# Performance work log

Hardware: AMD Instinct MI355X
Metric: run time of the kernel (lower is better)

## Reference

```python
import jax, jax.numpy as jnp
import numpy as np

RADIUS = 0.1          # acceptance_radius
CONF = 0.2            # confidence_threshold
MIN_LOCAL = 3         # min_local_correspondences
MIN_GLOBAL = 256      # min_global_correspondences
STEPS = 5             # num_refinement_steps
EPS = 1e-5
NTH = 8               # candidate thresholds CONF - 0.05*k (replaces data-dependent while loop)


def weighted_procrustes(src, tgt, w):
    """Weighted Kabsch. src/tgt: (..., N, 3), w: (..., N). Returns R (...,3,3), t (...,3)."""
    w = w / (jnp.sum(w, axis=-1, keepdims=True) + EPS)
    src_c = jnp.einsum('...n,...nc->...c', w, src)
    tgt_c = jnp.einsum('...n,...nc->...c', w, tgt)
    s0 = src - src_c[..., None, :]
    t0 = tgt - tgt_c[..., None, :]
    H = jnp.einsum('...nc,...n,...nd->...cd', s0, w, t0)  # (...,3,3)
    U, S, Vt = jnp.linalg.svd(H)
    V = jnp.swapaxes(Vt, -1, -2)
    det = jnp.linalg.det(jnp.matmul(V, jnp.swapaxes(U, -1, -2)))
    d = jnp.stack([jnp.ones_like(det), jnp.ones_like(det), det], axis=-1)
    R = jnp.einsum('...ik,...k,...jk->...ij', V, d, U)
    t = tgt_c - jnp.einsum('...ij,...j->...i', R, src_c)
    return R, t


def setup_inputs() -> dict:
    key = jax.random.key(0)
    k0, k1, k2 = jax.random.split(key, 3)
    B, K = 128, 64
    src = jax.random.normal(k0, (B, K, 3), dtype=jnp.float32)
    tgt = jax.random.normal(k1, (B, K, 3), dtype=jnp.float32)
    score_mat = jax.random.normal(k2, (B, K, K), dtype=jnp.float32) * 2.0 - 4.0
    src_masks = jnp.ones((B, K), dtype=bool)
    tgt_masks = jnp.ones((B, K), dtype=bool)
    return {
        'src_knn_points': src,
        'tgt_knn_points': tgt,
        'src_knn_masks': src_masks,
        'tgt_knn_masks': tgt_masks,
        'score_mat': score_mat,
    }


def reference(src_knn_points, tgt_knn_points, src_knn_masks, tgt_knn_masks, score_mat):
    B, K, _ = score_mat.shape
    score = jax.nn.sigmoid(score_mat)
    mask = src_knn_masks[:, :, None] & tgt_knn_masks[:, None, :]  # (B,K,K)

    # --- threshold search (dense replacement for the while loop) ---
    mg = jnp.minimum(min(3 * K, MIN_GLOBAL), jnp.sum(mask))
    th = CONF - 0.05 * jnp.arange(NTH, dtype=score.dtype)
    cnts = jnp.sum((score[None] > th[:, None, None, None]) & mask[None], axis=(1, 2, 3))
    thr = th[jnp.argmax(cnts >= mg)]  # first threshold with enough correspondences

    corr = (score > thr) & mask          # dense corr_mat (B,K,K)
    score = score * corr.astype(score.dtype)

    # --- dense (masked) correspondence batching: all (i,j) pairs per patch ---
    srcP = jnp.broadcast_to(src_knn_points[:, :, None, :], (B, K, K, 3)).reshape(B, K * K, 3)
    tgtP = jnp.broadcast_to(tgt_knn_points[:, None, :, :], (B, K, K, 3)).reshape(B, K * K, 3)
    w = score.reshape(B, K * K)

    # per-patch hypothesis transforms (zero-weight pairs are ignored by Procrustes)
    Rb, tb = weighted_procrustes(srcP, tgtP, w)  # (B,3,3), (B,3)
    counts_b = jnp.sum(corr, axis=(1, 2))
    valid = counts_b >= MIN_LOCAL

    # --- hypothesis verification: inlier counts over all global correspondences ---
    aligned = jnp.einsum('bxy,piy->bpix', Rb, src_knn_points) + tb[:, None, None, :]  # (B,B,K,3)
    cross = jnp.einsum('bpix,pjx->bpij', aligned, tgt_knn_points)                     # (B,B,K,K)
    res2 = (jnp.sum(aligned ** 2, -1)[..., None]
            + jnp.sum(tgt_knn_points ** 2, -1)[None, :, None, :]
            - 2.0 * cross)
    inlier = (res2 < RADIUS ** 2) & corr[None]                                        # (B,B,K,K)
    cnt_T = jnp.where(valid, jnp.sum(inlier, axis=(1, 2, 3)), -1)
    best = jnp.argmax(cnt_T)

    cur = score * inlier[best].astype(score.dtype)

    # --- global refinement ---
    src_all = srcP.reshape(-1, 3)
    tgt_all = tgtP.reshape(-1, 3)
    score_all = score.reshape(-1)
    R, t = weighted_procrustes(src_all, tgt_all, cur.reshape(-1))
    for _ in range(STEPS - 1):
        res = jnp.linalg.norm(tgt_all - (src_all @ R.T + t), axis=-1)
        cur_all = score_all * (res < RADIUS).astype(score.dtype)
        R, t = weighted_procrustes(src_all, tgt_all, cur_all)

    estimated_transform = jnp.eye(4, dtype=score.dtype).at[:3, :3].set(R).at[:3, 3].set(t)
    return estimated_transform, score  # score = dense-masked correspondence scores (B,K,K)
```

## Files before the change

### kernel.cpp

```cpp
#include <hip/hip_runtime.h>
#include <math.h>

#define BB   128
#define KK   64
#define K2   (KK*KK)
#define NTH  8
#define MG   192
#define MIN_LOCAL 3
#define RADIUS2 0.01f
#define RADIUSF 0.1f
#define NW   8

static constexpr size_t OFF_CNT8S = 0;
static constexpr size_t OFF_MA    = 0;
static constexpr size_t OFF_CNTU  = 8192;
static constexpr size_t OFF_MB    = 8192;
static constexpr size_t OFF_VALID = 40960;
static constexpr size_t OFF_RB    = 41472;
static constexpr size_t OFF_CB    = 47616;

__device__ inline void eigvec3(const double A[3][3], double lambda, double v[3]) {
    double r0x = A[0][0] - lambda, r0y = A[0][1], r0z = A[0][2];
    double r1x = A[0][1], r1y = A[1][1] - lambda, r1z = A[1][2];
    double r2x = A[0][2], r2y = A[1][2], r2z = A[2][2] - lambda;
    double c0x = r0y * r1z - r0z * r1y, c0y = r0z * r1x - r0x * r1z, c0z = r0x * r1y - r0y * r1x;
    double c1x = r0y * r2z - r0z * r2y, c1y = r0z * r2x - r0x * r2z, c1z = r0x * r2y - r0y * r2x;
    double c2x = r1y * r2z - r1z * r2y, c2y = r1z * r2x - r1x * r2z, c2z = r1x * r2y - r1y * r2x;
    double n0 = c0x * c0x + c0y * c0y + c0z * c0z;
    double n1 = c1x * c1x + c1y * c1y + c1z * c1z;
    double n2 = c2x * c2x + c2y * c2y + c2z * c2z;
    double bx = c0x, by = c0y, bz = c0z, nb = n0;
    if (n1 > nb) { bx = c1x; by = c1y; bz = c1z; nb = n1; }
    if (n2 > nb) { bx = c2x; by = c2y; bz = c2z; nb = n2; }
    if (nb < 1e-280) { v[0] = 1.0; v[1] = 0.0; v[2] = 0.0; return; }
    double s = 1.0 / sqrt(nb);
    v[0] = bx * s; v[1] = by * s; v[2] = bz * s;
}

__device__ inline void eig3(const double A[3][3], double V[3][3], double lam[3]) {
    double q = (A[0][0] + A[1][1] + A[2][2]) / 3.0;
    double a00 = A[0][0] - q, a11 = A[1][1] - q, a22 = A[2][2] - q;
    double p1 = A[0][1] * A[0][1] + A[0][2] * A[0][2] + A[1][2] * A[1][2];
    double p2 = a00 * a00 + a11 * a11 + a22 * a22 + 2.0 * p1;
    if (p2 < 1e-280) {
        lam[0] = q; lam[1] = q; lam[2] = q;
        for (int i = 0; i < 3; i++)
            for (int j = 0; j < 3; j++) V[i][j] = (i == j) ? 1.0 : 0.0;
        return;
    }
    double p = sqrt(p2 / 6.0);
    double ip = 1.0 / p;
    double b00 = a00 * ip, b11 = a11 * ip, b22 = a22 * ip;
    double b01 = A[0][1] * ip, b02 = A[0][2] * ip, b12 = A[1][2] * ip;
    double detB = b00 * (b11 * b22 - b12 * b12)
                - b01 * (b01 * b22 - b12 * b02)
                + b02 * (b01 * b12 - b11 * b02);
    double r = 0.5 * detB;
    r = fmin(1.0, fmax(-1.0, r));
    double phi = acos(r) / 3.0;
    double l0 = q + 2.0 * p * cos(phi);
    double l2 = q + 2.0 * p * cos(phi + 2.0943951023931953);
    double l1 = 3.0 * q - l0 - l2;
    lam[0] = l0; lam[1] = l1; lam[2] = l2;

    double v0[3], v2[3];
    eigvec3(A, l0, v0);
    eigvec3(A, l2, v2);
    double d = v0[0] * v2[0] + v0[1] * v2[1] + v0[2] * v2[2];
    v2[0] -= d * v0[0]; v2[1] -= d * v0[1]; v2[2] -= d * v0[2];
    double n = v2[0] * v2[0] + v2[1] * v2[1] + v2[2] * v2[2];
    if (n < 1e-280) {
        int k = (fabs(v0[0]) <= fabs(v0[1]) && fabs(v0[0]) <= fabs(v0[2])) ? 0
              : ((fabs(v0[1]) <= fabs(v0[2])) ? 1 : 2);
        double ax[3] = {0.0, 0.0, 0.0}; ax[k] = 1.0;
        double dd = v0[k];
        v2[0] = ax[0] - dd * v0[0]; v2[1] = ax[1] - dd * v0[1]; v2[2] = ax[2] - dd * v0[2];
        n = v2[0] * v2[0] + v2[1] * v2[1] + v2[2] * v2[2];
    }
    double s2 = 1.0 / sqrt(n);
    v2[0] *= s2; v2[1] *= s2; v2[2] *= s2;
    double v1[3] = { v2[1] * v0[2] - v2[2] * v0[1],
                     v2[2] * v0[0] - v2[0] * v0[2],
                     v2[0] * v0[1] - v2[1] * v0[0] };
    for (int i = 0; i < 3; i++) { V[i][0] = v0[i]; V[i][1] = v1[i]; V[i][2] = v2[i]; }
}

__device__ inline void kabsch_from_moments(const double* m, double R[3][3], double t[3]) {
    double W = m[0];
    double denom = W + 1e-5;
    double s = W / denom;
    double sc[3], tc[3];
    for (int c = 0; c < 3; c++) { sc[c] = m[1 + c] / denom; tc[c] = m[4 + c] / denom; }
    double H[3][3];
    for (int c = 0; c < 3; c++)
        for (int d = 0; d < 3; d++)
            H[c][d] = m[7 + c * 3 + d] / denom - (2.0 - s) * sc[c] * tc[d];
    double B3[3][3];
    for (int i = 0; i < 3; i++)
        for (int j = 0; j < 3; j++) {
            double v = 0.0;
            for (int k = 0; k < 3; k++) v += H[k][i] * H[k][j];
            B3[i][j] = v;
        }
    double V[3][3], lam[3];
    eig3(B3, V, lam);
    double inv[3];
    for (int k = 0; k < 3; k++) {
        double sg = sqrt(fmax(lam[k], 0.0));
        inv[k] = (sg > 1e-150) ? 1.0 / sg : 0.0;
    }
    double detH = H[0][0] * (H[1][1] * H[2][2] - H[1][2] * H[2][1])
                - H[0][1] * (H[1][0] * H[2][2] - H[1][2] * H[2][0])
                + H[0][2] * (H[1][0] * H[2][1] - H[1][1] * H[2][0]);
    if (detH < 0.0) inv[2] = -inv[2];
    double T2[3][3];
    for (int i = 0; i < 3; i++)
        for (int j = 0; j < 3; j++) {
            double v = 0.0;
            for (int k = 0; k < 3; k++) v += V[i][k] * inv[k] * V[j][k];
            T2[i][j] = v;
        }
    for (int i = 0; i < 3; i++)
        for (int j = 0; j < 3; j++) {
            double v = 0.0;
            for (int k = 0; k < 3; k++) v += T2[i][k] * H[j][k];
            R[i][j] = v;
        }
    for (int i = 0; i < 3; i++) {
        double v = tc[i];
        for (int j = 0; j < 3; j++) v -= R[i][j] * sc[j];
        t[i] = v;
    }
}

__global__ __launch_bounds__(512) void k_counts(
    const float* __restrict__ sm, int* __restrict__ cnt8s)
{
    const int t = threadIdx.x, lane = t & 63, wave = t >> 6;
    const int b = blockIdx.x;
    __shared__ int sC8[NTH];
    float xv[8];
    #pragma unroll
    for (int u = 0; u < 8; u++)
        xv[u] = sm[b * K2 + (u * NW + wave) * KK + lane];
    if (t < NTH) sC8[t] = 0;
    __syncthreads();
    int ck[NTH];
    #pragma unroll
    for (int k = 0; k < NTH; k++) ck[k] = 0;
    for (int u = 0; u < 8; u++) {
        float s = 1.0f / (1.0f + expf(-xv[u]));
        #pragma unroll
        for (int k = 0; k < NTH; k++) {
            unsigned long long bal = __ballot(s > (0.2f - 0.05f * (float)k));
            ck[k] += (int)__popcll(bal);
        }
    }
    if (lane == 0) {
        #pragma unroll
        for (int k = 0; k < NTH; k++) atomicAdd(&sC8[k], ck[k]);
    }
    __syncthreads();
    if (t < NTH) cnt8s[b * NTH + t] = sC8[t];
}

__global__ __launch_bounds__(512) void k_local(
    const float* __restrict__ src, const float* __restrict__ tgt,
    const float* __restrict__ sm, const int* __restrict__ cnt8s,
    float* __restrict__ score, unsigned long long* __restrict__ corrb,
    float* __restrict__ Rb, int* __restrict__ validA)
{
    const int t = threadIdx.x, lane = t & 63, wave = t >> 6;
    const int b = blockIdx.x;
    __shared__ float sS[192];
    __shared__ float sT[256];
    __shared__ float sRed[NW * 16];
    __shared__ int sRedi[NW];
    __shared__ float sThr;

    float xv[8];
    #pragma unroll
    for (int u = 0; u < 8; u++)
        xv[u] = sm[b * K2 + (u * NW + wave) * KK + lane];
    if (t < 192) sS[t] = src[b * 192 + t];
    if (t < 64) {
        float x = tgt[b * 192 + t * 3], y = tgt[b * 192 + t * 3 + 1], z = tgt[b * 192 + t * 3 + 2];
        sT[t * 4] = x; sT[t * 4 + 1] = y; sT[t * 4 + 2] = z; sT[t * 4 + 3] = x * x + y * y + z * z;
    }
    if (wave == 0) {
        int a[NTH];
        #pragma unroll
        for (int k = 0; k < NTH; k++)
            a[k] = cnt8s[lane * NTH + k] + cnt8s[(lane + 64) * NTH + k];
        #pragma unroll
        for (int off = 32; off; off >>= 1)
            #pragma unroll
            for (int k = 0; k < NTH; k++) a[k] += __shfl_down(a[k], off);
        if (lane == 0) {
            int kk2 = 0; bool found = false;
            #pragma unroll
            for (int k = 0; k < NTH; k++)
                if (!found && a[k] >= MG) { kk2 = k; found = true; }
            sThr = 0.2f - 0.05f * (float)kk2;
        }
    }
    __syncthreads();

    float thr = sThr;
    float tx0 = sT[lane * 4], ty0 = sT[lane * 4 + 1], tz0 = sT[lane * 4 + 2];
    float acc[16];
    #pragma unroll
    for (int k = 0; k < 16; k++) acc[k] = 0.0f;
    int cnt = 0;
    for (int u = 0; u < 8; u++) {
        int i = u * NW + wave;
        float s = 1.0f / (1.0f + expf(-xv[u]));
        bool c = (s > thr);
        float w = c ? s : 0.0f;
        score[b * K2 + i * KK + lane] = w;
        unsigned long long bal = __ballot(c);
        if (lane == 0) corrb[b * KK + i] = bal;
        cnt += c ? 1 : 0;
        float sx = sS[i * 3], sy = sS[i * 3 + 1], sz = sS[i * 3 + 2];
        acc[0]  += w;
        acc[1]  += w * sx; acc[2]  += w * sy; acc[3]  += w * sz;
        acc[4]  += w * tx0; acc[5]  += w * ty0; acc[6]  += w * tz0;
        acc[7]  += w * sx * tx0; acc[8]  += w * sx * ty0; acc[9]  += w * sx * tz0;
        acc[10] += w * sy * tx0; acc[11] += w * sy * ty0; acc[12] += w * sy * tz0;
        acc[13] += w * sz * tx0; acc[14] += w * sz * ty0; acc[15] += w * sz * tz0;
    }
    #pragma unroll
    for (int off = 32; off; off >>= 1) {
        #pragma unroll
        for (int k = 0; k < 16; k++) acc[k] += __shfl_down(acc[k], off);
        cnt += __shfl_down(cnt, off);
    }
    if (lane == 0) {
        for (int k = 0; k < 16; k++) sRed[wave * 16 + k] = acc[k];
        sRedi[wave] = cnt;
    }
    __syncthreads();
    if (t == 0) {
        double m[16];
        for (int k = 0; k < 16; k++) {
            float v = 0.0f;
            for (int wv = 0; wv < NW; wv++) v += sRed[wv * 16 + k];
            m[k] = (double)v;
        }
        double R[3][3], tv[3];
        kabsch_from_moments(m, R, tv);
        for (int i = 0; i < 3; i++)
            for (int j = 0; j < 3; j++) Rb[b * 12 + i * 3 + j] = (float)R[i][j];
        for (int i = 0; i < 3; i++) Rb[b * 12 + 9 + i] = (float)tv[i];
        int ctot = 0;
        for (int wv = 0; wv < NW; wv++) ctot += sRedi[wv];
        validA[b] = (ctot >= MIN_LOCAL) ? 1 : 0;
    }
}

__global__ __launch_bounds__(512) void k_verify(
    const float* __restrict__ src, const float* __restrict__ tgt,
    const unsigned long long* __restrict__ corrb, const float* __restrict__ Rb,
    unsigned int* __restrict__ cntU)
{
    const int t = threadIdx.x, lane = t & 63, wave = t >> 6;
    const int unit = blockIdx.x;
    const int p = unit >> 2, b0 = (unit & 3) * 32;
    __shared__ float sT[256];
    __shared__ float sRT[384];
    __shared__ int sCnt[32];

    if (t < 64) {
        float x = tgt[p * 192 + t * 3], y = tgt[p * 192 + t * 3 + 1], z = tgt[p * 192 + t * 3 + 2];
        sT[t * 4] = x; sT[t * 4 + 1] = y; sT[t * 4 + 2] = z; sT[t * 4 + 3] = x * x + y * y + z * z;
    }
    if (t < 384) sRT[t] = Rb[b0 * 12 + t];
    float sx = src[p * 192 + lane * 3];
    float sy = src[p * 192 + lane * 3 + 1];
    float sz = src[p * 192 + lane * 3 + 2];
    unsigned long long mask = corrb[p * KK + lane];
    __syncthreads();

    float ax[4], ay[4], az[4], sa[4];
    #pragma unroll
    for (int k = 0; k < 4; k++) {
        const float* RT = &sRT[(wave * 4 + k) * 12];
        ax[k] = RT[0] * sx + RT[1] * sy + RT[2] * sz + RT[9];
        ay[k] = RT[3] * sx + RT[4] * sy + RT[5] * sz + RT[10];
        az[k] = RT[6] * sx + RT[7] * sy + RT[8] * sz + RT[11];
        sa[k] = ax[k] * ax[k] + ay[k] * ay[k] + az[k] * az[k];
    }
    int c[4] = {0, 0, 0, 0};
    const float4* sT4 = (const float4*)sT;
    unsigned long long s = mask;
    while (s) {
        int j = (int)__builtin_ctzll(s);
        s &= s - 1ULL;
        float4 tv = sT4[j];
        #pragma unroll
        for (int k = 0; k < 4; k++) {
            float d2 = (sa[k] + tv.w) - 2.0f * (ax[k] * tv.x + ay[k] * tv.y + az[k] * tv.z);
            c[k] += (d2 < RADIUS2) ? 1 : 0;
        }
    }
    #pragma unroll
    for (int off = 32; off; off >>= 1)
        #pragma unroll
        for (int k = 0; k < 4; k++) c[k] += __shfl_down(c[k], off);
    if (lane == 0) {
        #pragma unroll
        for (int k = 0; k < 4; k++) sCnt[wave * 4 + k] = c[k];
    }
    __syncthreads();
    if (t < 16) {
        unsigned int pk = ((unsigned int)sCnt[2 * t] & 0xFFFFu)
                        | ((unsigned int)sCnt[2 * t + 1] << 16);
        cntU[unit * 16 + t] = pk;
    }
}

__device__ inline void refine_moments(
    const float* sS, const float* sT, const float* sRTf, float* sAl,
    const float* wv8, int t, int lane, int wave, bool it0,
    float* sRed)
{
    if (t < 64) {
        float x = sS[t * 3], y = sS[t * 3 + 1], z = sS[t * 3 + 2];
        float ax = sRTf[0] * x + sRTf[1] * y + sRTf[2] * z + sRTf[9];
        float ay = sRTf[3] * x + sRTf[4] * y + sRTf[5] * z + sRTf[10];
        float az = sRTf[6] * x + sRTf[7] * y + sRTf[8] * z + sRTf[11];
        sAl[t * 4] = ax; sAl[t * 4 + 1] = ay; sAl[t * 4 + 2] = az;
        sAl[t * 4 + 3] = ax * ax + ay * ay + az * az;
    }
    __syncthreads();
    float tx = sT[lane * 4], ty = sT[lane * 4 + 1], tz = sT[lane * 4 + 2], st2 = sT[lane * 4 + 3];
    float acc[16];
    #pragma unroll
    for (int k = 0; k < 16; k++) acc[k] = 0.0f;
    for (int u = 0; u < 8; u++) {
        int i = u * NW + wave;
        float sx = sS[i * 3], sy = sS[i * 3 + 1], sz = sS[i * 3 + 2];
        float ax = sAl[i * 4], ay = sAl[i * 4 + 1], az = sAl[i * 4 + 2], sa = sAl[i * 4 + 3];
        bool pred;
        if (it0) {
            float d2 = (sa + st2) - 2.0f * (ax * tx + ay * ty + az * tz);
            pred = (d2 < RADIUS2);
        } else {
            float dx = tx - ax, dy = ty - ay, dz = tz - az;
            pred = (sqrtf(dx * dx + dy * dy + dz * dz) < RADIUSF);
        }
        float w = wv8[u];
        float wf = pred ? w : 0.0f;
        acc[0]  += wf;
        acc[1]  += wf * sx; acc[2]  += wf * sy; acc[3]  += wf * sz;
        acc[4]  += wf * tx; acc[5]  += wf * ty; acc[6]  += wf * tz;
        acc[7]  += wf * sx * tx; acc[8]  += wf * sx * ty; acc[9]  += wf * sx * tz;
        acc[10] += wf * sy * tx; acc[11] += wf * sy * ty; acc[12] += wf * sy * tz;
        acc[13] += wf * sz * tx; acc[14] += wf * sz * ty; acc[15] += wf * sz * tz;
    }
    #pragma unroll
    for (int off = 32; off; off >>= 1)
        #pragma unroll
        for (int k = 0; k < 16; k++) acc[k] += __shfl_down(acc[k], off);
    if (lane == 0)
        for (int k = 0; k < 16; k++) sRed[wave * 16 + k] = acc[k];
}

__global__ __launch_bounds__(512) void k_sel_it0(
    const float* __restrict__ src, const float* __restrict__ tgt,
    const unsigned int* __restrict__ cntU, const int* __restrict__ validA,
    const float* __restrict__ Rb, const float* __restrict__ score,
    float* __restrict__ mout)
{
    const int t = threadIdx.x, lane = t & 63, wave = t >> 6;
    const int b = blockIdx.x;
    __shared__ float sS[192];
    __shared__ float sT[256];
    __shared__ float sAl[256];
    __shared__ float sRed[NW * 16];
    __shared__ int sCT[BB], sVv[BB];
    __shared__ int sCTp[512];
    __shared__ float sRTf[12];
    __shared__ int sBest;

    float wv8[8];
    #pragma unroll
    for (int u = 0; u < 8; u++)
        wv8[u] = score[b * K2 + (u * NW + wave) * KK + lane];
    if (t < 192) sS[t] = src[b * 192 + t];
    if (t < 64) {
        float x = tgt[b * 192 + t * 3], y = tgt[b * 192 + t * 3 + 1], z = tgt[b * 192 + t * 3 + 2];
        sT[t * 4] = x; sT[t * 4 + 1] = y; sT[t * 4 + 2] = z; sT[t * 4 + 3] = x * x + y * y + z * z;
    }
    {
        int q = t >> 7, h = t & 127;
        int g = h >> 5, w = (h & 31) >> 1, sh = (h & 1) * 16;
        int ssum = 0;
        for (int p = q * 32; p < q * 32 + 32; p++) {
            unsigned int wv = cntU[(p * 4 + g) * 16 + w];
            ssum += (int)((wv >> sh) & 0xFFFFu);
        }
        sCTp[t] = ssum;
    }
    __syncthreads();
    if (t < BB) {
        sCT[t] = sCTp[t] + sCTp[t + 128] + sCTp[t + 256] + sCTp[t + 384];
        sVv[t] = validA[t];
    }
    __syncthreads();
    if (t == 0) {
        int best = 0, bc = -2;
        for (int bb = 0; bb < BB; bb++) {
            int c = sVv[bb] ? sCT[bb] : -1;
            if (c > bc) { bc = c; best = bb; }
        }
        sBest = best;
    }
    __syncthreads();
    if (t < 12) sRTf[t] = Rb[sBest * 12 + t];
    __syncthreads();

    refine_moments(sS, sT, sRTf, sAl, wv8, t, lane, wave, true, sRed);
    __syncthreads();
    if (t < 16) {
        float v = 0.0f;
        for (int wv = 0; wv < NW; wv++) v += sRed[wv * 16 + t];
        mout[b * 16 + t] = v;
    }
}

__global__ __launch_bounds__(512) void k_refine(
    const float* __restrict__ src, const float* __restrict__ tgt,
    const float* __restrict__ score, const float* __restrict__ min_,
    float* __restrict__ mout)
{
    const int t = threadIdx.x, lane = t & 63, wave = t >> 6;
    const int b = blockIdx.x;
    __shared__ float sS[192];
    __shared__ float sT[256];
    __shared__ float sAl[256];
    __shared__ float sRed[NW * 16];
    __shared__ double sRTd[12];
    __shared__ float sRTf[12];

    float wv8[8];
    #pragma unroll
    for (int u = 0; u < 8; u++)
        wv8[u] = score[b * K2 + (u * NW + wave) * KK + lane];
    if (t < 192) sS[t] = src[b * 192 + t];
    if (t < 64) {
        float x = tgt[b * 192 + t * 3], y = tgt[b * 192 + t * 3 + 1], z = tgt[b * 192 + t * 3 + 2];
        sT[t * 4] = x; sT[t * 4 + 1] = y; sT[t * 4 + 2] = z; sT[t * 4 + 3] = x * x + y * y + z * z;
    }
    if (wave == 0) {
        double a[16];
        #pragma unroll
        for (int k = 0; k < 16; k++)
            a[k] = (double)min_[lane * 16 + k] + (double)min_[(lane + 64) * 16 + k];
        #pragma unroll
        for (int off = 32; off; off >>= 1)
            #pragma unroll
            for (int k = 0; k < 16; k++) a[k] += __shfl_down(a[k], off);
        if (lane == 0) {
            double R[3][3], tv[3];
            kabsch_from_moments(a, R, tv);
            for (int i = 0; i < 3; i++)
                for (int j = 0; j < 3; j++) sRTd[i * 3 + j] = R[i][j];
            for (int i = 0; i < 3; i++) sRTd[9 + i] = tv[i];
        }
    }
    __syncthreads();
    if (t < 12) sRTf[t] = (float)sRTd[t];
    __syncthreads();

    refine_moments(sS, sT, sRTf, sAl, wv8, t, lane, wave, false, sRed);
    __syncthreads();
    if (t < 16) {
        float v = 0.0f;
        for (int wv = 0; wv < NW; wv++) v += sRed[wv * 16 + t];
        mout[b * 16 + t] = v;
    }
}

__global__ __launch_bounds__(64) void k_final(
    const float* __restrict__ min_, float* __restrict__ out)
{
    const int lane = threadIdx.x;
    double a[16];
    #pragma unroll
    for (int k = 0; k < 16; k++)
        a[k] = (double)min_[lane * 16 + k] + (double)min_[(lane + 64) * 16 + k];
    #pragma unroll
    for (int off = 32; off; off >>= 1)
        #pragma unroll
        for (int k = 0; k < 16; k++) a[k] += __shfl_down(a[k], off);
    if (lane == 0) {
        double R[3][3], tv[3];
        kabsch_from_moments(a, R, tv);
        for (int i = 0; i < 3; i++) {
            for (int j = 0; j < 3; j++) out[i * 4 + j] = (float)R[i][j];
            out[i * 4 + 3] = (float)tv[i];
        }
        out[12] = 0.0f; out[13] = 0.0f; out[14] = 0.0f; out[15] = 1.0f;
    }
}

extern "C" void kernel_launch(void* const* d_in, const int* in_sizes, int n_in,
                              void* d_out, int out_size, void* d_ws, size_t ws_size,
                              hipStream_t stream) {
    const float* src = (const float*)d_in[0];
    const float* tgt = (const float*)d_in[1];
    const float* sm  = (const float*)d_in[4];
    float* out = (float*)d_out;
    char* ws = (char*)d_ws;

    int* cnt8s   = (int*)(ws + OFF_CNT8S);
    unsigned int* cntU = (unsigned int*)(ws + OFF_CNTU);
    float* mA    = (float*)(ws + OFF_MA);
    float* mB    = (float*)(ws + OFF_MB);
    int* validA  = (int*)(ws + OFF_VALID);
    float* Rb    = (float*)(ws + OFF_RB);
    unsigned long long* corrb = (unsigned long long*)(ws + OFF_CB);
    float* score = out + 16;

    k_counts <<<BB, 512, 0, stream>>>(sm, cnt8s);
    k_local  <<<BB, 512, 0, stream>>>(src, tgt, sm, cnt8s, score, corrb, Rb, validA);
    k_verify <<<512, 512, 0, stream>>>(src, tgt, corrb, Rb, cntU);
    k_sel_it0<<<BB, 512, 0, stream>>>(src, tgt, cntU, validA, Rb, score, mA);
    k_refine <<<BB, 512, 0, stream>>>(src, tgt, score, mA, mB);
    k_refine <<<BB, 512, 0, stream>>>(src, tgt, score, mB, mA);
    k_refine <<<BB, 512, 0, stream>>>(src, tgt, score, mA, mB);
    k_refine <<<BB, 512, 0, stream>>>(src, tgt, score, mB, mA);
    k_final  <<<1, 64, 0, stream>>>(mA, out);
}
```

Before: 145.0 us.

## Fuse refinement iterations into one persistent kernel with grid-wide spin barriers

Replaces the selection kernel, the four refine launches and the final reduction with a single 8-block persistent kernel. Each block handles 16 batches and publishes per-iteration moment sums through atomics and tags. All blocks spin-wait on those tags, then recompute Kabsch redundantly. This removes about six kernel launches and their gaps, at the cost of using only 8 CUs for the refinement work. It also relies on all 8 blocks being co-resident and on a timeout-guarded spin barrier.

New measurement: 364.4 us. 2.51x slower.

```diff
diff --git a/kernel.cpp b/kernel.cpp
--- a/kernel.cpp
+++ b/kernel.cpp
@@ -10,14 +10,16 @@
 #define RADIUS2 0.01f
 #define RADIUSF 0.1f
 #define NW   8
+#define NRB  8
+#define AGT  __HIP_MEMORY_SCOPE_AGENT
 
 static constexpr size_t OFF_CNT8S = 0;
-static constexpr size_t OFF_MA    = 0;
-static constexpr size_t OFF_CNTU  = 8192;
-static constexpr size_t OFF_MB    = 8192;
-static constexpr size_t OFF_VALID = 40960;
-static constexpr size_t OFF_RB    = 41472;
-static constexpr size_t OFF_CB    = 47616;
+static constexpr size_t OFF_CNTU  = 4096;
+static constexpr size_t OFF_VALID = 36864;
+static constexpr size_t OFF_RB    = 37376;
+static constexpr size_t OFF_CB    = 43520;
+static constexpr size_t OFF_TAGR  = 109056;
+static constexpr size_t OFF_MSD   = 109120;
 
 __device__ inline void eigvec3(const double A[3][3], double lambda, double v[3]) {
     double r0x = A[0][0] - lambda, r0y = A[0][1], r0z = A[0][2];
@@ -131,6 +133,23 @@
         for (int j = 0; j < 3; j++) v -= R[i][j] * sc[j];
         t[i] = v;
     }
+}
+
+__device__ inline void wait8(const int* tagR, int lane, int val) {
+    int spins = 0;
+    unsigned long long t0 = 0;
+    for (;;) {
+        bool ok = (lane >= NRB) ||
+                  (__hip_atomic_load(&tagR[lane], __ATOMIC_RELAXED, AGT) >= val);
+        if (__ballot(ok) == ~0ULL) break;
+        if (spins > 16) __builtin_amdgcn_s_sleep(1);
+        if ((++spins & 63) == 0) {
+            unsigned long long now = __builtin_amdgcn_s_memrealtime();
+            if (t0 == 0) t0 = now;
+            else if (__ballot(now - t0 > 10000000ULL) != 0ULL) break;
+        }
+    }
+    __atomic_signal_fence(__ATOMIC_SEQ_CST);
 }
 
 __global__ __launch_bounds__(512) void k_counts(
@@ -261,7 +280,7 @@
 __global__ __launch_bounds__(512) void k_verify(
     const float* __restrict__ src, const float* __restrict__ tgt,
     const unsigned long long* __restrict__ corrb, const float* __restrict__ Rb,
-    unsigned int* __restrict__ cntU)
+    unsigned int* __restrict__ cntU, int* __restrict__ tagR)
 {
     const int t = threadIdx.x, lane = t & 63, wave = t >> 6;
     const int unit = blockIdx.x;
@@ -270,6 +289,7 @@
     __shared__ float sRT[384];
     __shared__ int sCnt[32];
 
+    if (unit == 0 && t < 16) tagR[t] = 0;
     if (t < 64) {
         float x = tgt[p * 192 + t * 3], y = tgt[p * 192 + t * 3 + 1], z = tgt[p * 192 + t * 3 + 2];
         sT[t * 4] = x; sT[t * 4 + 1] = y; sT[t * 4 + 2] = z; sT[t * 4 + 3] = x * x + y * y + z * z;
@@ -319,79 +339,37 @@
     }
 }
 
-__device__ inline void refine_moments(
-    const float* sS, const float* sT, const float* sRTf, float* sAl,
-    const float* wv8, int t, int lane, int wave, bool it0,
-    float* sRed)
-{
-    if (t < 64) {
-        float x = sS[t * 3], y = sS[t * 3 + 1], z = sS[t * 3 + 2];
-        float ax = sRTf[0] * x + sRTf[1] * y + sRTf[2] * z + sRTf[9];
-        float ay = sRTf[3] * x + sRTf[4] * y + sRTf[5] * z + sRTf[10];
-        float az = sRTf[6] * x + sRTf[7] * y + sRTf[8] * z + sRTf[11];
-        sAl[t * 4] = ax; sAl[t * 4 + 1] = ay; sAl[t * 4 + 2] = az;
-        sAl[t * 4 + 3] = ax * ax + ay * ay + az * az;
-    }
-    __syncthreads();
-    float tx = sT[lane * 4], ty = sT[lane * 4 + 1], tz = sT[lane * 4 + 2], st2 = sT[lane * 4 + 3];
-    float acc[16];
-    #pragma unroll
-    for (int k = 0; k < 16; k++) acc[k] = 0.0f;
-    for (int u = 0; u < 8; u++) {
-        int i = u * NW + wave;
-        float sx = sS[i * 3], sy = sS[i * 3 + 1], sz = sS[i * 3 + 2];
-        float ax = sAl[i * 4], ay = sAl[i * 4 + 1], az = sAl[i * 4 + 2], sa = sAl[i * 4 + 3];
-        bool pred;
-        if (it0) {
-            float d2 = (sa + st2) - 2.0f * (ax * tx + ay * ty + az * tz);
-            pred = (d2 < RADIUS2);
-        } else {
-            float dx = tx - ax, dy = ty - ay, dz = tz - az;
-            pred = (sqrtf(dx * dx + dy * dy + dz * dz) < RADIUSF);
-        }
-        float w = wv8[u];
-        float wf = pred ? w : 0.0f;
-        acc[0]  += wf;
-        acc[1]  += wf * sx; acc[2]  += wf * sy; acc[3]  += wf * sz;
-        acc[4]  += wf * tx; acc[5]  += wf * ty; acc[6]  += wf * tz;
-        acc[7]  += wf * sx * tx; acc[8]  += wf * sx * ty; acc[9]  += wf * sx * tz;
-        acc[10] += wf * sy * tx; acc[11] += wf * sy * ty; acc[12] += wf * sy * tz;
-        acc[13] += wf * sz * tx; acc[14] += wf * sz * ty; acc[15] += wf * sz * tz;
-    }
-    #pragma unroll
-    for (int off = 32; off; off >>= 1)
-        #pragma unroll
-        for (int k = 0; k < 16; k++) acc[k] += __shfl_down(acc[k], off);
-    if (lane == 0)
-        for (int k = 0; k < 16; k++) sRed[wave * 16 + k] = acc[k];
-}
-
-__global__ __launch_bounds__(512) void k_sel_it0(
+__global__ __launch_bounds__(512) void k_refineall(
     const float* __restrict__ src, const float* __restrict__ tgt,
-    const unsigned int* __restrict__ cntU, const int* __restrict__ validA,
-    const float* __restrict__ Rb, const float* __restrict__ score,
-    float* __restrict__ mout)
+    const float* __restrict__ score, const unsigned int* __restrict__ cntU,
+    const int* __restrict__ validA, const float* __restrict__ Rb,
+    int* __restrict__ tagR, double* __restrict__ msd, float* __restrict__ out)
 {
     const int t = threadIdx.x, lane = t & 63, wave = t >> 6;
-    const int b = blockIdx.x;
-    __shared__ float sS[192];
-    __shared__ float sT[256];
-    __shared__ float sAl[256];
-    __shared__ float sRed[NW * 16];
+    const int blk = blockIdx.x;
+
+    __shared__ float sSp[16 * 192];
+    __shared__ float sTp[16 * 256];
+    __shared__ float sAl[16 * 256];
+    __shared__ float sRedAll[16 * 8 * 16];
+    __shared__ float sPm[16 * 16];
+    __shared__ double sMdL[16];
     __shared__ int sCT[BB], sVv[BB];
     __shared__ int sCTp[512];
+    __shared__ double sRTd[12];
     __shared__ float sRTf[12];
     __shared__ int sBest;
 
-    float wv8[8];
-    #pragma unroll
-    for (int u = 0; u < 8; u++)
-        wv8[u] = score[b * K2 + (u * NW + wave) * KK + lane];
-    if (t < 192) sS[t] = src[b * 192 + t];
-    if (t < 64) {
-        float x = tgt[b * 192 + t * 3], y = tgt[b * 192 + t * 3 + 1], z = tgt[b * 192 + t * 3 + 2];
-        sT[t * 4] = x; sT[t * 4 + 1] = y; sT[t * 4 + 2] = z; sT[t * 4 + 3] = x * x + y * y + z * z;
-    }
+    for (int idx = t; idx < 16 * 192; idx += 512)
+        sSp[idx] = src[blk * 16 * 192 + idx];
+    for (int idx = t; idx < 1024; idx += 512) {
+        int p = idx >> 6, i = idx & 63;
+        const float* tp = tgt + (blk * 16 + p) * 192 + i * 3;
+        float x = tp[0], y = tp[1], z = tp[2];
+        sTp[idx * 4] = x; sTp[idx * 4 + 1] = y; sTp[idx * 4 + 2] = z;
+        sTp[idx * 4 + 3] = x * x + y * y + z * z;
+    }
+
     {
         int q = t >> 7, h = t & 127;
         int g = h >> 5, w = (h & 31) >> 1, sh = (h & 1) * 16;
@@ -420,88 +398,119 @@
     if (t < 12) sRTf[t] = Rb[sBest * 12 + t];
     __syncthreads();
 
-    refine_moments(sS, sT, sRTf, sAl, wv8, t, lane, wave, true, sRed);
-    __syncthreads();
-    if (t < 16) {
-        float v = 0.0f;
-        for (int wv = 0; wv < NW; wv++) v += sRed[wv * 16 + t];
-        mout[b * 16 + t] = v;
-    }
-}
-
-__global__ __launch_bounds__(512) void k_refine(
-    const float* __restrict__ src, const float* __restrict__ tgt,
-    const float* __restrict__ score, const float* __restrict__ min_,
-    float* __restrict__ mout)
-{
-    const int t = threadIdx.x, lane = t & 63, wave = t >> 6;
-    const int b = blockIdx.x;
-    __shared__ float sS[192];
-    __shared__ float sT[256];
-    __shared__ float sAl[256];
-    __shared__ float sRed[NW * 16];
-    __shared__ double sRTd[12];
-    __shared__ float sRTf[12];
-
-    float wv8[8];
-    #pragma unroll
-    for (int u = 0; u < 8; u++)
-        wv8[u] = score[b * K2 + (u * NW + wave) * KK + lane];
-    if (t < 192) sS[t] = src[b * 192 + t];
-    if (t < 64) {
-        float x = tgt[b * 192 + t * 3], y = tgt[b * 192 + t * 3 + 1], z = tgt[b * 192 + t * 3 + 2];
-        sT[t * 4] = x; sT[t * 4 + 1] = y; sT[t * 4 + 2] = z; sT[t * 4 + 3] = x * x + y * y + z * z;
-    }
-    if (wave == 0) {
-        double a[16];
-        #pragma unroll
-        for (int k = 0; k < 16; k++)
-            a[k] = (double)min_[lane * 16 + k] + (double)min_[(lane + 64) * 16 + k];
-        #pragma unroll
-        for (int off = 32; off; off >>= 1)
+    for (int it = 0; it < 5; it++) {
+        for (int idx = t; idx < 1024; idx += 512) {
+            int p = idx >> 6, i = idx & 63;
+            float x = sSp[p * 192 + i * 3], y = sSp[p * 192 + i * 3 + 1], z = sSp[p * 192 + i * 3 + 2];
+            float ax = sRTf[0] * x + sRTf[1] * y + sRTf[2] * z + sRTf[9];
+            float ay = sRTf[3] * x + sRTf[4] * y + sRTf[5] * z + sRTf[10];
+            float az = sRTf[6] * x + sRTf[7] * y + sRTf[8] * z + sRTf[11];
+            sAl[idx * 4] = ax; sAl[idx * 4 + 1] = ay; sAl[idx * 4 + 2] = az;
+            sAl[idx * 4 + 3] = ax * ax + ay * ay + az * az;
+        }
+        __syncthreads();
+        for (int p = 0; p < 16; p++) {
+            float tx = sTp[(p * 64 + lane) * 4],     ty = sTp[(p * 64 + lane) * 4 + 1];
+            float tz = sTp[(p * 64 + lane) * 4 + 2], st2 = sTp[(p * 64 + lane) * 4 + 3];
+            const float* scp = score + (blk * 16 + p) * K2;
+            float acc[16];
             #pragma unroll
-            for (int k = 0; k < 16; k++) a[k] += __shfl_down(a[k], off);
-        if (lane == 0) {
-            double R[3][3], tv[3];
-            kabsch_from_moments(a, R, tv);
-            for (int i = 0; i < 3; i++)
-                for (int j = 0; j < 3; j++) sRTd[i * 3 + j] = R[i][j];
-            for (int i = 0; i < 3; i++) sRTd[9 + i] = tv[i];
-        }
-    }
-    __syncthreads();
-    if (t < 12) sRTf[t] = (float)sRTd[t];
-    __syncthreads();
-
-    refine_moments(sS, sT, sRTf, sAl, wv8, t, lane, wave, false, sRed);
-    __syncthreads();
-    if (t < 16) {
-        float v = 0.0f;
-        for (int wv = 0; wv < NW; wv++) v += sRed[wv * 16 + t];
-        mout[b * 16 + t] = v;
-    }
-}
-
-__global__ __launch_bounds__(64) void k_final(
-    const float* __restrict__ min_, float* __restrict__ out)
-{
-    const int lane = threadIdx.x;
-    double a[16];
-    #pragma unroll
-    for (int k = 0; k < 16; k++)
-        a[k] = (double)min_[lane * 16 + k] + (double)min_[(lane + 64) * 16 + k];
-    #pragma unroll
-    for (int off = 32; off; off >>= 1)
-        #pragma unroll
-        for (int k = 0; k < 16; k++) a[k] += __shfl_down(a[k], off);
-    if (lane == 0) {
-        double R[3][3], tv[3];
-        kabsch_from_moments(a, R, tv);
-        for (int i = 0; i < 3; i++) {
-            for (int j = 0; j < 3; j++) out[i * 4 + j] = (float)R[i][j];
-            out[i * 4 + 3] = (float)tv[i];
-        }
-        out[12] = 0.0f; out[13] = 0.0f; out[14] = 0.0f; out[15] = 1.0f;
+            for (int k = 0; k < 16; k++) acc[k] = 0.0f;
+            for (int u = 0; u < 8; u++) {
+                int i = u * NW + wave;
+                float w = scp[i * KK + lane];
+                float sx = sSp[p * 192 + i * 3], sy = sSp[p * 192 + i * 3 + 1], sz = sSp[p * 192 + i * 3 + 2];
+                int ai = (p * 64 + i) * 4;
+                float ax = sAl[ai], ay = sAl[ai + 1], az = sAl[ai + 2], sa = sAl[ai + 3];
+                bool pred;
+                if (it == 0) {
+                    float d2 = (sa + st2) - 2.0f * (ax * tx + ay * ty + az * tz);
+                    pred = (d2 < RADIUS2);
+                } else {
+                    float dx = tx - ax, dy = ty - ay, dz = tz - az;
+                    pred = (sqrtf(dx * dx + dy * dy + dz * dz) < RADIUSF);
+                }
+                float wf = pred ? w : 0.0f;
+                acc[0]  += wf;
+                acc[1]  += wf * sx; acc[2]  += wf * sy; acc[3]  += wf * sz;
+                acc[4]  += wf * tx; acc[5]  += wf * ty; acc[6]  += wf * tz;
+                acc[7]  += wf * sx * tx; acc[8]  += wf * sx * ty; acc[9]  += wf * sx * tz;
+                acc[10] += wf * sy * tx; acc[11] += wf * sy * ty; acc[12] += wf * sy * tz;
+                acc[13] += wf * sz * tx; acc[14] += wf * sz * ty; acc[15] += wf * sz * tz;
+            }
+            #pragma unroll
+            for (int off = 32; off; off >>= 1)
+                #pragma unroll
+                for (int k = 0; k < 16; k++) acc[k] += __shfl_down(acc[k], off);
+            if (lane == 0)
+                for (int k = 0; k < 16; k++) sRedAll[(p * 8 + wave) * 16 + k] = acc[k];
+        }
+        __syncthreads();
+        if (t < 256) {
+            int p = t >> 4, k = t & 15;
+            float v = 0.0f;
+            for (int wv = 0; wv < NW; wv++) v += sRedAll[(p * 8 + wv) * 16 + k];
+            sPm[p * 16 + k] = v;
+        }
+        __syncthreads();
+        int par = it & 1;
+        if (t < 16) {
+            double md = 0.0;
+            for (int p = 0; p < 16; p++) md += (double)sPm[p * 16 + t];
+            __hip_atomic_store(&msd[(par * NRB + blk) * 16 + t], md, __ATOMIC_RELAXED, AGT);
+        }
+        __syncthreads();
+        if (t == 0)
+            __hip_atomic_store(&tagR[blk], it + 1, __ATOMIC_RELEASE, AGT);
+
+        if (it < 4) {
+            if (wave == 0) wait8(tagR, lane, it + 1);
+            __syncthreads();
+            if (t < 16) {
+                double md = 0.0;
+                #pragma unroll
+                for (int b2 = 0; b2 < NRB; b2++)
+                    md += __hip_atomic_load(&msd[(par * NRB + b2) * 16 + t], __ATOMIC_RELAXED, AGT);
+                sMdL[t] = md;
+            }
+            __syncthreads();
+            if (t == 0) {
+                double m[16];
+                for (int k = 0; k < 16; k++) m[k] = sMdL[k];
+                double R[3][3], tv[3];
+                kabsch_from_moments(m, R, tv);
+                for (int i = 0; i < 3; i++)
+                    for (int jj = 0; jj < 3; jj++) sRTd[i * 3 + jj] = R[i][jj];
+                for (int i = 0; i < 3; i++) sRTd[9 + i] = tv[i];
+            }
+            __syncthreads();
+            if (t < 12) sRTf[t] = (float)sRTd[t];
+            __syncthreads();
+        } else {
+            if (blk != 0) return;
+            if (wave == 0) wait8(tagR, lane, 5);
+            __syncthreads();
+            if (t < 16) {
+                double md = 0.0;
+                #pragma unroll
+                for (int b2 = 0; b2 < NRB; b2++)
+                    md += __hip_atomic_load(&msd[(par * NRB + b2) * 16 + t], __ATOMIC_RELAXED, AGT);
+                sMdL[t] = md;
+            }
+            __syncthreads();
+            if (t == 0) {
+                double m[16];
+                for (int k = 0; k < 16; k++) m[k] = sMdL[k];
+                double R[3][3], tv[3];
+                kabsch_from_moments(m, R, tv);
+                for (int i = 0; i < 3; i++) {
+                    for (int jj = 0; jj < 3; jj++) out[i * 4 + jj] = (float)R[i][jj];
+                    out[i * 4 + 3] = (float)tv[i];
+                }
+                out[12] = 0.0f; out[13] = 0.0f; out[14] = 0.0f; out[15] = 1.0f;
+            }
+            return;
+        }
     }
 }
 
@@ -516,20 +525,15 @@
 
     int* cnt8s   = (int*)(ws + OFF_CNT8S);
     unsigned int* cntU = (unsigned int*)(ws + OFF_CNTU);
-    float* mA    = (float*)(ws + OFF_MA);
-    float* mB    = (float*)(ws + OFF_MB);
     int* validA  = (int*)(ws + OFF_VALID);
     float* Rb    = (float*)(ws + OFF_RB);
     unsigned long long* corrb = (unsigned long long*)(ws + OFF_CB);
+    int* tagR    = (int*)(ws + OFF_TAGR);
+    double* msd  = (double*)(ws + OFF_MSD);
     float* score = out + 16;
 
-    k_counts <<<BB, 512, 0, stream>>>(sm, cnt8s);
-    k_local  <<<BB, 512, 0, stream>>>(src, tgt, sm, cnt8s, score, corrb, Rb, validA);
-    k_verify <<<512, 512, 0, stream>>>(src, tgt, corrb, Rb, cntU);
-    k_sel_it0<<<BB, 512, 0, stream>>>(src, tgt, cntU, validA, Rb, score, mA);
-    k_refine <<<BB, 512, 0, stream>>>(src, tgt, score, mA, mB);
-    k_refine <<<BB, 512, 0, stream>>>(src, tgt, score, mB, mA);
-    k_refine <<<BB, 512, 0, stream>>>(src, tgt, score, mA, mB);
-    k_refine <<<BB, 512, 0, stream>>>(src, tgt, score, mB, mA);
-    k_final  <<<1, 64, 0, stream>>>(mA, out);
-}
+    k_counts   <<<BB, 512, 0, stream>>>(sm, cnt8s);
+    k_local    <<<BB, 512, 0, stream>>>(src, tgt, sm, cnt8s, score, corrb, Rb, validA);
+    k_verify   <<<512, 512, 0, stream>>>(src, tgt, corrb, Rb, cntU, tagR);
+    k_refineall<<<NRB, 512, 0, stream>>>(src, tgt, score, cntU, validA, Rb, tagR, msd, out);
+}
```

## Speculate threshold 0.2 and drop count kernel, with single-block fallback recompute

Applied to the files above, without the earlier changes.

Removes the separate threshold-counting kernel. The local stage now assumes the threshold is 0.2 and computes the per-threshold counts alongside its other work. The real threshold is resolved in the verify kernel and checked in the final kernel. If the guess was wrong, a single 512-thread block redoes the local, verify and refine stages serially. This saves one launch and a global sync on the common path, but the fallback path would be extremely slow.

After: 143.6 us. Within noise of the previous version (-1.0%).

```diff
diff --git a/kernel.cpp b/kernel.cpp
--- a/kernel.cpp
+++ b/kernel.cpp
@@ -12,12 +12,13 @@
 #define NW   8
 
 static constexpr size_t OFF_CNT8S = 0;
-static constexpr size_t OFF_MA    = 0;
-static constexpr size_t OFF_CNTU  = 8192;
-static constexpr size_t OFF_MB    = 8192;
-static constexpr size_t OFF_VALID = 40960;
-static constexpr size_t OFF_RB    = 41472;
-static constexpr size_t OFF_CB    = 47616;
+static constexpr size_t OFF_CNTU  = 4096;
+static constexpr size_t OFF_CB    = 36864;
+static constexpr size_t OFF_MA    = 36864;
+static constexpr size_t OFF_MB    = 45056;
+static constexpr size_t OFF_VALID = 102400;
+static constexpr size_t OFF_RB    = 102912;
+static constexpr size_t OFF_THR   = 109056;
 
 __device__ inline void eigvec3(const double A[3][3], double lambda, double v[3]) {
     double r0x = A[0][0] - lambda, r0y = A[0][1], r0z = A[0][2];
@@ -133,42 +134,11 @@
     }
 }
 
-__global__ __launch_bounds__(512) void k_counts(
-    const float* __restrict__ sm, int* __restrict__ cnt8s)
-{
-    const int t = threadIdx.x, lane = t & 63, wave = t >> 6;
-    const int b = blockIdx.x;
-    __shared__ int sC8[NTH];
-    float xv[8];
-    #pragma unroll
-    for (int u = 0; u < 8; u++)
-        xv[u] = sm[b * K2 + (u * NW + wave) * KK + lane];
-    if (t < NTH) sC8[t] = 0;
-    __syncthreads();
-    int ck[NTH];
-    #pragma unroll
-    for (int k = 0; k < NTH; k++) ck[k] = 0;
-    for (int u = 0; u < 8; u++) {
-        float s = 1.0f / (1.0f + expf(-xv[u]));
-        #pragma unroll
-        for (int k = 0; k < NTH; k++) {
-            unsigned long long bal = __ballot(s > (0.2f - 0.05f * (float)k));
-            ck[k] += (int)__popcll(bal);
-        }
-    }
-    if (lane == 0) {
-        #pragma unroll
-        for (int k = 0; k < NTH; k++) atomicAdd(&sC8[k], ck[k]);
-    }
-    __syncthreads();
-    if (t < NTH) cnt8s[b * NTH + t] = sC8[t];
-}
-
-__global__ __launch_bounds__(512) void k_local(
+__global__ __launch_bounds__(512) void k_local_f(
     const float* __restrict__ src, const float* __restrict__ tgt,
-    const float* __restrict__ sm, const int* __restrict__ cnt8s,
-    float* __restrict__ score, unsigned long long* __restrict__ corrb,
-    float* __restrict__ Rb, int* __restrict__ validA)
+    const float* __restrict__ sm, float* __restrict__ score,
+    unsigned long long* __restrict__ corrb, float* __restrict__ Rb,
+    int* __restrict__ validA, int* __restrict__ cnt8s)
 {
     const int t = threadIdx.x, lane = t & 63, wave = t >> 6;
     const int b = blockIdx.x;
@@ -176,7 +146,7 @@
     __shared__ float sT[256];
     __shared__ float sRed[NW * 16];
     __shared__ int sRedi[NW];
-    __shared__ float sThr;
+    __shared__ int sC8[NTH];
 
     float xv[8];
     #pragma unroll
@@ -187,34 +157,26 @@
         float x = tgt[b * 192 + t * 3], y = tgt[b * 192 + t * 3 + 1], z = tgt[b * 192 + t * 3 + 2];
         sT[t * 4] = x; sT[t * 4 + 1] = y; sT[t * 4 + 2] = z; sT[t * 4 + 3] = x * x + y * y + z * z;
     }
-    if (wave == 0) {
-        int a[NTH];
-        #pragma unroll
-        for (int k = 0; k < NTH; k++)
-            a[k] = cnt8s[lane * NTH + k] + cnt8s[(lane + 64) * NTH + k];
-        #pragma unroll
-        for (int off = 32; off; off >>= 1)
-            #pragma unroll
-            for (int k = 0; k < NTH; k++) a[k] += __shfl_down(a[k], off);
-        if (lane == 0) {
-            int kk2 = 0; bool found = false;
-            #pragma unroll
-            for (int k = 0; k < NTH; k++)
-                if (!found && a[k] >= MG) { kk2 = k; found = true; }
-            sThr = 0.2f - 0.05f * (float)kk2;
-        }
-    }
-    __syncthreads();
-
-    float thr = sThr;
+    if (t < NTH) sC8[t] = 0;
+    __syncthreads();
+
+    const float thr = 0.2f;
     float tx0 = sT[lane * 4], ty0 = sT[lane * 4 + 1], tz0 = sT[lane * 4 + 2];
     float acc[16];
     #pragma unroll
     for (int k = 0; k < 16; k++) acc[k] = 0.0f;
     int cnt = 0;
+    int ck[NTH];
+    #pragma unroll
+    for (int k = 0; k < NTH; k++) ck[k] = 0;
     for (int u = 0; u < 8; u++) {
         int i = u * NW + wave;
         float s = 1.0f / (1.0f + expf(-xv[u]));
+        #pragma unroll
+        for (int k = 0; k < NTH; k++) {
+            unsigned long long balk = __ballot(s > (0.2f - 0.05f * (float)k));
+            ck[k] += (int)__popcll(balk);
+        }
         bool c = (s > thr);
         float w = c ? s : 0.0f;
         score[b * K2 + i * KK + lane] = w;
@@ -229,6 +191,10 @@
         acc[10] += w * sy * tx0; acc[11] += w * sy * ty0; acc[12] += w * sy * tz0;
         acc[13] += w * sz * tx0; acc[14] += w * sz * ty0; acc[15] += w * sz * tz0;
     }
+    if (lane == 0) {
+        #pragma unroll
+        for (int k = 0; k < NTH; k++) atomicAdd(&sC8[k], ck[k]);
+    }
     #pragma unroll
     for (int off = 32; off; off >>= 1) {
         #pragma unroll
@@ -240,6 +206,7 @@
         sRedi[wave] = cnt;
     }
     __syncthreads();
+    if (t < NTH) cnt8s[b * NTH + t] = sC8[t];
     if (t == 0) {
         double m[16];
         for (int k = 0; k < 16; k++) {
@@ -261,7 +228,8 @@
 __global__ __launch_bounds__(512) void k_verify(
     const float* __restrict__ src, const float* __restrict__ tgt,
     const unsigned long long* __restrict__ corrb, const float* __restrict__ Rb,
-    unsigned int* __restrict__ cntU)
+    const int* __restrict__ cnt8s, unsigned int* __restrict__ cntU,
+    float* __restrict__ thrp)
 {
     const int t = threadIdx.x, lane = t & 63, wave = t >> 6;
     const int unit = blockIdx.x;
@@ -270,6 +238,23 @@
     __shared__ float sRT[384];
     __shared__ int sCnt[32];
 
+    if (unit == 0 && wave == 0) {
+        int a[NTH];
+        #pragma unroll
+        for (int k = 0; k < NTH; k++)
+            a[k] = cnt8s[lane * NTH + k] + cnt8s[(lane + 64) * NTH + k];
+        #pragma unroll
+        for (int off = 32; off; off >>= 1)
+            #pragma unroll
+            for (int k = 0; k < NTH; k++) a[k] += __shfl_down(a[k], off);
+        if (lane == 0) {
+            int kk2 = 0; bool found = false;
+            #pragma unroll
+            for (int k = 0; k < NTH; k++)
+                if (!found && a[k] >= MG) { kk2 = k; found = true; }
+            thrp[0] = 0.2f - 0.05f * (float)kk2;
+        }
+    }
     if (t < 64) {
         float x = tgt[p * 192 + t * 3], y = tgt[p * 192 + t * 3 + 1], z = tgt[p * 192 + t * 3 + 2];
         sT[t * 4] = x; sT[t * 4 + 1] = y; sT[t * 4 + 2] = z; sT[t * 4 + 3] = x * x + y * y + z * z;
@@ -482,26 +467,192 @@
     }
 }
 
-__global__ __launch_bounds__(64) void k_final(
-    const float* __restrict__ min_, float* __restrict__ out)
+__global__ __launch_bounds__(512) void k_final(
+    const float* __restrict__ src, const float* __restrict__ tgt,
+    const float* __restrict__ sm, const float* __restrict__ min_,
+    const float* __restrict__ thrp, float* __restrict__ score,
+    float* __restrict__ out)
 {
-    const int lane = threadIdx.x;
-    double a[16];
-    #pragma unroll
-    for (int k = 0; k < 16; k++)
-        a[k] = (double)min_[lane * 16 + k] + (double)min_[(lane + 64) * 16 + k];
-    #pragma unroll
-    for (int off = 32; off; off >>= 1)
-        #pragma unroll
-        for (int k = 0; k < 16; k++) a[k] += __shfl_down(a[k], off);
-    if (lane == 0) {
-        double R[3][3], tv[3];
-        kabsch_from_moments(a, R, tv);
-        for (int i = 0; i < 3; i++) {
-            for (int j = 0; j < 3; j++) out[i * 4 + j] = (float)R[i][j];
-            out[i * 4 + 3] = (float)tv[i];
-        }
-        out[12] = 0.0f; out[13] = 0.0f; out[14] = 0.0f; out[15] = 1.0f;
+    const int t = threadIdx.x, lane = t & 63, wave = t >> 6;
+    __shared__ float sS[192];
+    __shared__ float sT[256];
+    __shared__ float sAl[256];
+    __shared__ float sRed[NW * 16];
+    __shared__ int sRedi[NW];
+    __shared__ double sRTd[12];
+    __shared__ float sRTf[12];
+    __shared__ float cRbF[BB * 12];
+    __shared__ int cValid[BB];
+    __shared__ int cCnt[BB];
+    __shared__ double gM[16];
+    __shared__ int sBestC;
+
+    const float thr_real = thrp[0];
+    if (thr_real == 0.2f) {
+        if (wave == 0) {
+            double a[16];
+            #pragma unroll
+            for (int k = 0; k < 16; k++)
+                a[k] = (double)min_[lane * 16 + k] + (double)min_[(lane + 64) * 16 + k];
+            #pragma unroll
+            for (int off = 32; off; off >>= 1)
+                #pragma unroll
+                for (int k = 0; k < 16; k++) a[k] += __shfl_down(a[k], off);
+            if (lane == 0) {
+                double R[3][3], tv[3];
+                kabsch_from_moments(a, R, tv);
+                for (int i = 0; i < 3; i++) {
+                    for (int j = 0; j < 3; j++) out[i * 4 + j] = (float)R[i][j];
+                    out[i * 4 + 3] = (float)tv[i];
+                }
+                out[12] = 0.0f; out[13] = 0.0f; out[14] = 0.0f; out[15] = 1.0f;
+            }
+        }
+        return;
+    }
+
+    const float thr = thr_real;
+    for (int p = 0; p < BB; p++) {
+        __syncthreads();
+        if (t < 192) sS[t] = src[p * 192 + t];
+        if (t < 64) {
+            float x = tgt[p * 192 + t * 3], y = tgt[p * 192 + t * 3 + 1], z = tgt[p * 192 + t * 3 + 2];
+            sT[t * 4] = x; sT[t * 4 + 1] = y; sT[t * 4 + 2] = z; sT[t * 4 + 3] = x * x + y * y + z * z;
+        }
+        __syncthreads();
+        float tx0 = sT[lane * 4], ty0 = sT[lane * 4 + 1], tz0 = sT[lane * 4 + 2];
+        float acc[16];
+        #pragma unroll
+        for (int k = 0; k < 16; k++) acc[k] = 0.0f;
+        int cnt = 0;
+        for (int u = 0; u < 8; u++) {
+            int i = u * NW + wave;
+            float s = 1.0f / (1.0f + expf(-sm[p * K2 + i * KK + lane]));
+            bool c = (s > thr);
+            float w = c ? s : 0.0f;
+            score[p * K2 + i * KK + lane] = w;
+            cnt += c ? 1 : 0;
+            float sx = sS[i * 3], sy = sS[i * 3 + 1], sz = sS[i * 3 + 2];
+            acc[0]  += w;
+            acc[1]  += w * sx; acc[2]  += w * sy; acc[3]  += w * sz;
+            acc[4]  += w * tx0; acc[5]  += w * ty0; acc[6]  += w * tz0;
+            acc[7]  += w * sx * tx0; acc[8]  += w * sx * ty0; acc[9]  += w * sx * tz0;
+            acc[10] += w * sy * tx0; acc[11] += w * sy * ty0; acc[12] += w * sy * tz0;
+            acc[13] += w * sz * tx0; acc[14] += w * sz * ty0; acc[15] += w * sz * tz0;
+        }
+        #pragma unroll
+        for (int off = 32; off; off >>= 1) {
+            #pragma unroll
+            for (int k = 0; k < 16; k++) acc[k] += __shfl_down(acc[k], off);
+            cnt += __shfl_down(cnt, off);
+        }
+        if (lane == 0) {
+            for (int k = 0; k < 16; k++) sRed[wave * 16 + k] = acc[k];
+            sRedi[wave] = cnt;
+        }
+        __syncthreads();
+        if (t == 0) {
+            double m[16];
+            for (int k = 0; k < 16; k++) {
+                float v = 0.0f;
+                for (int wv = 0; wv < NW; wv++) v += sRed[wv * 16 + k];
+                m[k] = (double)v;
+            }
+            double R[3][3], tv[3];
+            kabsch_from_moments(m, R, tv);
+            for (int i = 0; i < 3; i++)
+                for (int j = 0; j < 3; j++) cRbF[p * 12 + i * 3 + j] = (float)R[i][j];
+            for (int i = 0; i < 3; i++) cRbF[p * 12 + 9 + i] = (float)tv[i];
+            int ctot = 0;
+            for (int wv = 0; wv < NW; wv++) ctot += sRedi[wv];
+            cValid[p] = (ctot >= MIN_LOCAL) ? 1 : 0;
+        }
+    }
+    __syncthreads();
+    if (t < BB) cCnt[t] = 0;
+    __syncthreads();
+    for (int p = 0; p < BB; p++) {
+        if (t < 192) sS[t] = src[p * 192 + t];
+        if (t < 64) {
+            float x = tgt[p * 192 + t * 3], y = tgt[p * 192 + t * 3 + 1], z = tgt[p * 192 + t * 3 + 2];
+            sT[t * 4] = x; sT[t * 4 + 1] = y; sT[t * 4 + 2] = z; sT[t * 4 + 3] = x * x + y * y + z * z;
+        }
+        __syncthreads();
+        for (int rep = 0; rep < 8; rep++) {
+            int idx = rep * 512 + t, i = idx >> 6, j = idx & 63;
+            float w = score[p * K2 + i * KK + j];
+            if (w > 0.0f) {
+                float sx = sS[i * 3], sy = sS[i * 3 + 1], sz = sS[i * 3 + 2];
+                float tx = sT[j * 4], ty = sT[j * 4 + 1], tz = sT[j * 4 + 2], st2 = sT[j * 4 + 3];
+                for (int h = 0; h < BB; h++) {
+                    const float* RT = &cRbF[h * 12];
+                    float ax = RT[0] * sx + RT[1] * sy + RT[2] * sz + RT[9];
+                    float ay = RT[3] * sx + RT[4] * sy + RT[5] * sz + RT[10];
+                    float az = RT[6] * sx + RT[7] * sy + RT[8] * sz + RT[11];
+                    float d2 = (ax * ax + ay * ay + az * az + st2)
+                             - 2.0f * (ax * tx + ay * ty + az * tz);
+                    if (d2 < RADIUS2) atomicAdd(&cCnt[h], 1);
+                }
+            }
+        }
+        __syncthreads();
+    }
+    if (t == 0) {
+        int best = 0, bc = -2;
+        for (int bb = 0; bb < BB; bb++) {
+            int c = cValid[bb] ? cCnt[bb] : -1;
+            if (c > bc) { bc = c; best = bb; }
+        }
+        sBestC = best;
+    }
+    __syncthreads();
+    if (t < 12) sRTf[t] = cRbF[sBestC * 12 + t];
+    __syncthreads();
+    for (int it = 0; it < 5; it++) {
+        if (t < 16) gM[t] = 0.0;
+        __syncthreads();
+        for (int p = 0; p < BB; p++) {
+            if (t < 192) sS[t] = src[p * 192 + t];
+            if (t < 64) {
+                float x = tgt[p * 192 + t * 3], y = tgt[p * 192 + t * 3 + 1], z = tgt[p * 192 + t * 3 + 2];
+                sT[t * 4] = x; sT[t * 4 + 1] = y; sT[t * 4 + 2] = z; sT[t * 4 + 3] = x * x + y * y + z * z;
+            }
+            __syncthreads();
+            float wv8[8];
+            #pragma unroll
+            for (int u = 0; u < 8; u++)
+                wv8[u] = score[p * K2 + (u * NW + wave) * KK + lane];
+            refine_moments(sS, sT, sRTf, sAl, wv8, t, lane, wave, it == 0, sRed);
+            __syncthreads();
+            if (t < 16) {
+                float v = 0.0f;
+                for (int wv = 0; wv < NW; wv++) v += sRed[wv * 16 + t];
+                gM[t] += (double)v;
+            }
+            __syncthreads();
+        }
+        if (t == 0) {
+            double m[16];
+            for (int k = 0; k < 16; k++) m[k] = gM[k];
+            double R[3][3], tv[3];
+            kabsch_from_moments(m, R, tv);
+            if (it < 4) {
+                for (int i = 0; i < 3; i++)
+                    for (int j = 0; j < 3; j++) sRTd[i * 3 + j] = R[i][j];
+                for (int i = 0; i < 3; i++) sRTd[9 + i] = tv[i];
+            } else {
+                for (int i = 0; i < 3; i++) {
+                    for (int j = 0; j < 3; j++) out[i * 4 + j] = (float)R[i][j];
+                    out[i * 4 + 3] = (float)tv[i];
+                }
+                out[12] = 0.0f; out[13] = 0.0f; out[14] = 0.0f; out[15] = 1.0f;
+            }
+        }
+        __syncthreads();
+        if (it < 4) {
+            if (t < 12) sRTf[t] = (float)sRTd[t];
+            __syncthreads();
+        }
     }
 }
 
@@ -516,20 +667,20 @@
 
     int* cnt8s   = (int*)(ws + OFF_CNT8S);
     unsigned int* cntU = (unsigned int*)(ws + OFF_CNTU);
+    unsigned long long* corrb = (unsigned long long*)(ws + OFF_CB);
     float* mA    = (float*)(ws + OFF_MA);
     float* mB    = (float*)(ws + OFF_MB);
     int* validA  = (int*)(ws + OFF_VALID);
     float* Rb    = (float*)(ws + OFF_RB);
-    unsigned long long* corrb = (unsigned long long*)(ws + OFF_CB);
+    float* thrp  = (float*)(ws + OFF_THR);
     float* score = out + 16;
 
-    k_counts <<<BB, 512, 0, stream>>>(sm, cnt8s);
-    k_local  <<<BB, 512, 0, stream>>>(src, tgt, sm, cnt8s, score, corrb, Rb, validA);
-    k_verify <<<512, 512, 0, stream>>>(src, tgt, corrb, Rb, cntU);
+    k_local_f<<<BB, 512, 0, stream>>>(src, tgt, sm, score, corrb, Rb, validA, cnt8s);
+    k_verify <<<512, 512, 0, stream>>>(src, tgt, corrb, Rb, cnt8s, cntU, thrp);
     k_sel_it0<<<BB, 512, 0, stream>>>(src, tgt, cntU, validA, Rb, score, mA);
     k_refine <<<BB, 512, 0, stream>>>(src, tgt, score, mA, mB);
     k_refine <<<BB, 512, 0, stream>>>(src, tgt, score, mB, mA);
     k_refine <<<BB, 512, 0, stream>>>(src, tgt, score, mA, mB);
     k_refine <<<BB, 512, 0, stream>>>(src, tgt, score, mB, mA);
-    k_final  <<<1, 64, 0, stream>>>(mA, out);
-}
+    k_final  <<<1, 512, 0, stream>>>(src, tgt, sm, mA, thrp, score, out);
+}
```
